# Optimization experiments

Measured on AMD Instinct MI355X. Metric: run time of the kernel, lower is better.

## Reference

```python
import jax, jax.numpy as jnp
import numpy as np

HEADS = 1
WC = 32  # weight_channels (weights shared across channel groups via c % WC)
K1 = 3
K2 = 5
PAD1 = 1
PAD2 = 2


def _patches(x, k, pad):
    # x: [N, C, H, W] -> [N, C, k*k, H, W], zero padding, stride 1, dilation 1
    N, C, H, W = x.shape
    xp = jnp.pad(x, ((0, 0), (0, 0), (pad, pad), (pad, pad)))
    ps = [xp[:, :, i:i + H, j:j + W] for i in range(k) for j in range(k)]
    return jnp.stack(ps, axis=2)


def setup_inputs() -> dict:
    key = jax.random.key(0)
    k1, k2 = jax.random.split(key)
    x = jax.random.normal(k1, (2, 256, 64, 64), dtype=jnp.float32)
    # weight layout: [N, heads*WC*(K1*K1 + K2*K2), H, W] = [2, 1*32*(9+25), 64, 64]
    weight = jax.random.normal(k2, (2, HEADS * WC * (K1 * K1 + K2 * K2), 64, 64), dtype=jnp.float32)
    return {"x": x, "weight": weight}


def reference(x, weight):
    N, C, H, W = x.shape
    g = C // WC  # channel groups sharing the same per-pixel weights
    n1 = HEADS * WC * K1 * K1
    w1 = weight[:, :n1].reshape(N, HEADS, WC, K1 * K1, H, W)
    w2 = weight[:, n1:].reshape(N, HEADS, WC, K2 * K2, H, W)

    p1 = _patches(x, K1, PAD1).reshape(N, g, WC, K1 * K1, H, W)
    p2 = _patches(x, K2, PAD2).reshape(N, g, WC, K2 * K2, H, W)

    out1 = jnp.einsum('ngckhw,nackhw->nagchw', p1, w1).reshape(N, HEADS, C, H, W)
    out2 = jnp.einsum('ngckhw,nackhw->nagchw', p2, w2).reshape(N, HEADS, C, H, W)
    # top layout: [N, kernel_num=2, heads, C, H, W]
    return jnp.stack([out1, out2], axis=1)
```

## Files before the change

kernel.cpp:

```cpp
#include <hip/hip_runtime.h>


#define HW_ 4096

__device__ __forceinline__ float dpp_shl1(float v) {
  return __builtin_bit_cast(
      float, __builtin_amdgcn_update_dpp(0, __builtin_bit_cast(int, v),
                                         0x130, 0xF, 0xF, true));
}
__device__ __forceinline__ float dpp_shr1(float v) {
  return __builtin_bit_cast(
      float, __builtin_amdgcn_update_dpp(0, __builtin_bit_cast(int, v),
                                         0x138, 0xF, 0xF, true));
}

__global__ __launch_bounds__(256) void lconv_mix_kernel(
    const float* __restrict__ x, const float* __restrict__ wgt,
    float* __restrict__ out) {
  int idx = blockIdx.x * blockDim.x + threadIdx.x;
  int w  = idx & 63;
  int h  = (idx >> 6) & 63;
  int wc = (idx >> 12) & 31;
  int n  = idx >> 17;

  const float* wbase = wgt + (size_t)n * 1088 * HW_ + h * 64 + w;
  float w1[9], w2[25];
#pragma unroll
  for (int t = 0; t < 9; ++t)
    w1[t] = __builtin_nontemporal_load(&wbase[(size_t)(wc * 9 + t) * HW_]);
#pragma unroll
  for (int t = 0; t < 25; ++t)
    w2[t] = __builtin_nontemporal_load(&wbase[(size_t)(288 + wc * 25 + t) * HW_]);

  const float* xn = x + (size_t)n * 256 * HW_ + h * 64 + w;
  float* o1 = out + ((size_t)(n * 2 + 0) * 256) * HW_ + h * 64 + w;
  float* o2 = out + ((size_t)(n * 2 + 1) * 256) * HW_ + h * 64 + w;

#pragma unroll
  for (int g = 0; g < 8; ++g) {
    int cc = g * 32 + wc;
    const float* xc = xn + (size_t)cc * HW_;

    float r[5];
#pragma unroll
    for (int i = 0; i < 5; ++i) {
      int hh = h + i - 2;
      r[i] = ((unsigned)hh < 64u) ? xc[(i - 2) * 64] : 0.0f;
    }

    float a1 = 0.0f, a2 = 0.0f;
#pragma unroll
    for (int i = 0; i < 5; ++i) {
      float m1 = dpp_shr1(r[i]);
      float m2 = dpp_shr1(m1);
      float q1 = dpp_shl1(r[i]);
      float q2 = dpp_shl1(q1);

      a2 = fmaf(m2,   w2[i * 5 + 0], a2);
      a2 = fmaf(m1,   w2[i * 5 + 1], a2);
      a2 = fmaf(r[i], w2[i * 5 + 2], a2);
      a2 = fmaf(q1,   w2[i * 5 + 3], a2);
      a2 = fmaf(q2,   w2[i * 5 + 4], a2);

      if (i >= 1 && i <= 3) {
        a1 = fmaf(m1,   w1[(i - 1) * 3 + 0], a1);
        a1 = fmaf(r[i], w1[(i - 1) * 3 + 1], a1);
        a1 = fmaf(q1,   w1[(i - 1) * 3 + 2], a1);
      }
    }

    __builtin_nontemporal_store(a1, &o1[(size_t)cc * HW_]);
    __builtin_nontemporal_store(a2, &o2[(size_t)cc * HW_]);
  }
}

extern "C" void kernel_launch(void* const* d_in, const int* in_sizes, int n_in,
                              void* d_out, int out_size, void* d_ws,
                              size_t ws_size, hipStream_t stream) {
  const float* x = (const float*)d_in[0];
  const float* wgt = (const float*)d_in[1];
  float* out = (float*)d_out;

  int total = 2 * 32 * 64 * 64;
  lconv_mix_kernel<<<dim3(total / 256), dim3(256), 0, stream>>>(x, wgt, out);
}
```

Measured before the change: 93.05 us.

## Process four pixels per thread with float4 loads and row-level DPP shifts

Each thread now computes four adjacent pixels. Weights, inputs and outputs move as 16-byte vectors, and the horizontal neighbours come from row_shl/row_shr DPP, so 16 lanes cover one 64-pixel image row. This cuts the number of memory instructions and DPP ops per output. The cost is a four-times smaller grid of only 256 blocks, about one block per CU, plus much higher register use from 34 float4 weights. That may hurt latency hiding.

```diff
diff --git a/kernel.cpp b/kernel.cpp
--- a/kernel.cpp
+++ b/kernel.cpp
@@ -2,75 +2,84 @@
 
 
 #define HW_ 4096
+typedef float f4 __attribute__((ext_vector_type(4)));
 
-__device__ __forceinline__ float dpp_shl1(float v) {
+__device__ __forceinline__ float row_shl1(float v) {
   return __builtin_bit_cast(
       float, __builtin_amdgcn_update_dpp(0, __builtin_bit_cast(int, v),
-                                         0x130, 0xF, 0xF, true));
+                                         0x101, 0xF, 0xF, true));
 }
-__device__ __forceinline__ float dpp_shr1(float v) {
+__device__ __forceinline__ float row_shr1(float v) {
   return __builtin_bit_cast(
       float, __builtin_amdgcn_update_dpp(0, __builtin_bit_cast(int, v),
-                                         0x138, 0xF, 0xF, true));
+                                         0x111, 0xF, 0xF, true));
 }
 
-__global__ __launch_bounds__(256) void lconv_mix_kernel(
+__device__ __forceinline__ void fma4(f4& acc, f4 a, f4 b) {
+  acc.x = fmaf(a.x, b.x, acc.x);
+  acc.y = fmaf(a.y, b.y, acc.y);
+  acc.z = fmaf(a.z, b.z, acc.z);
+  acc.w = fmaf(a.w, b.w, acc.w);
+}
+
+__global__ __launch_bounds__(256, 1) void lconv_mix_kernel(
     const float* __restrict__ x, const float* __restrict__ wgt,
     float* __restrict__ out) {
-  int idx = blockIdx.x * blockDim.x + threadIdx.x;
-  int w  = idx & 63;
-  int h  = (idx >> 6) & 63;
-  int wc = (idx >> 12) & 31;
-  int n  = idx >> 17;
+  int idx = blockIdx.x * 256 + threadIdx.x;
+  int h  = (idx >> 4) & 63;
+  int wc = (idx >> 10) & 31;
+  int n  = idx >> 15;
+  int pix = (idx & 0x3FF) << 2;
 
-  const float* wbase = wgt + (size_t)n * 1088 * HW_ + h * 64 + w;
-  float w1[9], w2[25];
+  const f4* wb = (const f4*)(wgt + (size_t)n * 1088 * HW_ + pix);
+  f4 w1[9], w2[25];
 #pragma unroll
   for (int t = 0; t < 9; ++t)
-    w1[t] = __builtin_nontemporal_load(&wbase[(size_t)(wc * 9 + t) * HW_]);
+    w1[t] = __builtin_nontemporal_load(&wb[(size_t)(wc * 9 + t) * 1024]);
 #pragma unroll
   for (int t = 0; t < 25; ++t)
-    w2[t] = __builtin_nontemporal_load(&wbase[(size_t)(288 + wc * 25 + t) * HW_]);
+    w2[t] = __builtin_nontemporal_load(&wb[(size_t)(288 + wc * 25 + t) * 1024]);
 
-  const float* xn = x + (size_t)n * 256 * HW_ + h * 64 + w;
-  float* o1 = out + ((size_t)(n * 2 + 0) * 256) * HW_ + h * 64 + w;
-  float* o2 = out + ((size_t)(n * 2 + 1) * 256) * HW_ + h * 64 + w;
+  const float* xn = x + (size_t)n * 256 * HW_ + pix;
+  float* o1 = out + ((size_t)(n * 2 + 0) * 256) * HW_ + pix;
+  float* o2 = out + ((size_t)(n * 2 + 1) * 256) * HW_ + pix;
 
 #pragma unroll
   for (int g = 0; g < 8; ++g) {
     int cc = g * 32 + wc;
-    const float* xc = xn + (size_t)cc * HW_;
+    const f4* xc = (const f4*)(xn + (size_t)cc * HW_);
 
-    float r[5];
+    f4 a1 = {0.f, 0.f, 0.f, 0.f}, a2 = {0.f, 0.f, 0.f, 0.f};
 #pragma unroll
     for (int i = 0; i < 5; ++i) {
       int hh = h + i - 2;
-      r[i] = ((unsigned)hh < 64u) ? xc[(i - 2) * 64] : 0.0f;
-    }
+      f4 v = {0.f, 0.f, 0.f, 0.f};
+      if ((unsigned)hh < 64u) v = xc[(i - 2) * 16];
 
-    float a1 = 0.0f, a2 = 0.0f;
-#pragma unroll
-    for (int i = 0; i < 5; ++i) {
-      float m1 = dpp_shr1(r[i]);
-      float m2 = dpp_shr1(m1);
-      float q1 = dpp_shl1(r[i]);
-      float q2 = dpp_shl1(q1);
+      float lx = row_shr1(v.w);
+      float lz = row_shr1(v.z);
+      float rx = row_shl1(v.x);
+      float ry = row_shl1(v.y);
+      f4 m1 = {lx, v.x, v.y, v.z};
+      f4 m2 = {lz, lx, v.x, v.y};
+      f4 q1 = {v.y, v.z, v.w, rx};
+      f4 q2 = {v.z, v.w, rx, ry};
 
-      a2 = fmaf(m2,   w2[i * 5 + 0], a2);
-      a2 = fmaf(m1,   w2[i * 5 + 1], a2);
-      a2 = fmaf(r[i], w2[i * 5 + 2], a2);
-      a2 = fmaf(q1,   w2[i * 5 + 3], a2);
-      a2 = fmaf(q2,   w2[i * 5 + 4], a2);
+      fma4(a2, m2, w2[i * 5 + 0]);
+      fma4(a2, m1, w2[i * 5 + 1]);
+      fma4(a2, v,  w2[i * 5 + 2]);
+      fma4(a2, q1, w2[i * 5 + 3]);
+      fma4(a2, q2, w2[i * 5 + 4]);
 
       if (i >= 1 && i <= 3) {
-        a1 = fmaf(m1,   w1[(i - 1) * 3 + 0], a1);
-        a1 = fmaf(r[i], w1[(i - 1) * 3 + 1], a1);
-        a1 = fmaf(q1,   w1[(i - 1) * 3 + 2], a1);
+        fma4(a1, m1, w1[(i - 1) * 3 + 0]);
+        fma4(a1, v,  w1[(i - 1) * 3 + 1]);
+        fma4(a1, q1, w1[(i - 1) * 3 + 2]);
       }
     }
 
-    __builtin_nontemporal_store(a1, &o1[(size_t)cc * HW_]);
-    __builtin_nontemporal_store(a2, &o2[(size_t)cc * HW_]);
+    __builtin_nontemporal_store(a1, (f4*)(o1 + (size_t)cc * HW_));
+    __builtin_nontemporal_store(a2, (f4*)(o2 + (size_t)cc * HW_));
   }
 }
 
@@ -81,6 +90,6 @@
   const float* wgt = (const float*)d_in[1];
   float* out = (float*)d_out;
 
-  int total = 2 * 32 * 64 * 64;
+  int total = 2 * 32 * 64 * 16;
   lconv_mix_kernel<<<dim3(total / 256), dim3(256), 0, stream>>>(x, wgt, out);
 }
```

New measurement: 99.29 us. 6.7% more time.
